# Optimization experiments

Hardware: AMD Instinct MI355X
Metric: run time of the kernel (lower is better)

## Reference

```python
import jax, jax.numpy as jnp
import numpy as np

N = 10000
E = 320000
IN = 10000
HID = 128
NCLS = 2


def setup_inputs() -> dict:
    key = jax.random.key(0)
    ks = jax.random.split(key, 8)
    x = jax.random.normal(ks[0], (N, IN), dtype=jnp.float32)
    edge_index = jax.random.randint(ks[1], (2, E), 0, N, dtype=jnp.int64)
    edge_weight = jax.random.uniform(ks[2], (E,), dtype=jnp.float32)
    # GCNConv linear (no bias folding issues: PyG GCNConv uses Linear(in, out, bias=False) + separate bias)
    W_conv = jax.random.normal(ks[3], (IN, HID), dtype=jnp.float32) / np.sqrt(IN)
    b_conv = jnp.zeros((HID,), dtype=jnp.float32)
    W_lin = jax.random.normal(ks[4], (HID, NCLS), dtype=jnp.float32) / np.sqrt(HID)
    b_lin = jnp.zeros((NCLS,), dtype=jnp.float32)
    return {"x": x, "edge_index": edge_index, "edge_weight": edge_weight,
            "W_conv": W_conv, "b_conv": b_conv, "W_lin": W_lin, "b_lin": b_lin}


def reference(x, edge_index, edge_weight, W_conv, b_conv, W_lin, b_lin):
    n = x.shape[0]
    row, col = edge_index[0], edge_index[1]
    # add self loops with weight 1 (GCNConv add_self_loops=True, fill_value=1.)
    loop = jnp.arange(n, dtype=row.dtype)
    row = jnp.concatenate([row, loop])
    col = jnp.concatenate([col, loop])
    ew = jnp.concatenate([edge_weight, jnp.ones((n,), dtype=edge_weight.dtype)])
    # symmetric GCN normalization: deg from destination (col) index
    deg = jax.ops.segment_sum(ew, col, num_segments=n)
    dinv = jnp.where(deg > 0, jax.lax.rsqrt(deg), 0.0)
    norm = dinv[row] * ew * dinv[col]  # [E+N]
    # linear transform then weighted scatter-add aggregation
    h = x @ W_conv                      # [N, HID]
    msg = norm[:, None] * h[row]        # [E+N, HID] gather on source nodes
    out = jax.ops.segment_sum(msg, col, num_segments=n) + b_conv  # [N, HID]
    out = jax.nn.relu(out)
    # dropout p=0.0 is identity
    logits = out @ W_lin + b_lin        # [N, 2]
    return jax.nn.softmax(logits, axis=1)
```

## Files before the change

### kernel.cpp

```cpp
#include <hip/hip_runtime.h>
#include <hip/hip_bf16.h>
#include <math.h>

#define NN   10000
#define NE   320000
#define KK   10000
#define HID  128
#define KPAD 10048
#define MT   79
#define KITERS 157
#define NSPLIT 8

typedef __bf16 bf16x8 __attribute__((ext_vector_type(8)));
typedef float  f32x16 __attribute__((ext_vector_type(16)));

#define OFF_DINV 0u
#define OFF_FLAG 40960u
#define OFF_CNT  45056u
#define OFF_ROW  86016u
#define OFF_CUR  126976u
#define OFF_ER   262144u
#define OFF_EC   1572864u
#define OFF_CSRS 2883584u
#define OFF_CSRW 4194304u
#define OFF_H    8388608u
#define OFF_WT   13631488u

__device__ inline unsigned short f2bf(float f) {
  unsigned int v = __builtin_bit_cast(unsigned int, f);
  unsigned int lsb = (v >> 16) & 1u;
  v += 0x7fffu + lsb;
  return (unsigned short)(v >> 16);
}

__global__ __launch_bounds__(64) void k_detect(const int* __restrict__ ei,
                                               int* __restrict__ flag) {
  int t = threadIdx.x;
  int v = ei[2*t + 1];
  unsigned long long b = __ballot(v != 0);
  if (t == 0) flag[0] = (b == 0ull) ? 1 : 0;
}

__global__ __launch_bounds__(256) void k_edges(const int* __restrict__ ei,
                                               const int* __restrict__ flag,
                                               int* __restrict__ er,
                                               int* __restrict__ ec) {
  int e = blockIdx.x*256 + threadIdx.x;
  if (e < NE) {
    int s = flag[0];
    er[e] = ei[(size_t)e << s];
    ec[e] = ei[((size_t)(NE + e)) << s];
  }
}

__global__ __launch_bounds__(256) void k_transpose(const float* __restrict__ W,
                                                   unsigned short* __restrict__ Wt) {
  __shared__ float t[32][33];
  const int tx = threadIdx.x, ty = threadIdx.y;
  const int bk = blockIdx.x, bn = blockIdx.y;
#pragma unroll
  for (int j = 0; j < 4; ++j) {
    int k = bk*32 + ty + j*8;
    int n = bn*32 + tx;
    float v = 0.0f;
    if (k < KK) v = W[(size_t)k*HID + n];
    t[ty + j*8][tx] = v;
  }
  __syncthreads();
#pragma unroll
  for (int j = 0; j < 4; ++j) {
    int n = bn*32 + ty + j*8;
    int k = bk*32 + tx;
    Wt[(size_t)n*KPAD + k] = f2bf(t[tx][ty + j*8]);
  }
}

__global__ __launch_bounds__(256) void k_deg(const int* __restrict__ ec,
                                             const float* __restrict__ ew,
                                             float* __restrict__ deg,
                                             int* __restrict__ cnt) {
  int e = blockIdx.x*256 + threadIdx.x;
  if (e < NE) {
    int c = ec[e];
    atomicAdd(&deg[c], ew[e]);
    atomicAdd(&cnt[c], 1);
  }
}

__global__ __launch_bounds__(256) void k_dinv(float* __restrict__ deg) {
  int i = blockIdx.x*256 + threadIdx.x;
  if (i < NN) {
    float d = deg[i] + 1.0f;
    deg[i] = (d > 0.0f) ? (1.0f / sqrtf(d)) : 0.0f;
  }
}

__global__ __launch_bounds__(256) void k_scan(const int* __restrict__ cnt,
                                              int* __restrict__ rowstart,
                                              int* __restrict__ cursor) {
  __shared__ int sums[256];
  const int t = threadIdx.x;
  const int CH = 40;
  const int base = t * CH;
  int s = 0;
  for (int k = 0; k < CH; ++k) {
    int i = base + k;
    if (i < NN) s += cnt[i];
  }
  sums[t] = s;
  __syncthreads();
  for (int off = 1; off < 256; off <<= 1) {
    int add = (t >= off) ? sums[t - off] : 0;
    __syncthreads();
    sums[t] += add;
    __syncthreads();
  }
  int run = (t == 0) ? 0 : sums[t - 1];
  for (int k = 0; k < CH; ++k) {
    int i = base + k;
    if (i < NN) {
      rowstart[i] = run;
      cursor[i]   = run;
      run += cnt[i];
    }
  }
  if (t == 255) rowstart[NN] = run;
}

__global__ __launch_bounds__(256) void k_scatter(const int* __restrict__ er,
                                                 const int* __restrict__ ec,
                                                 const float* __restrict__ ew,
                                                 const float* __restrict__ dinv,
                                                 int* __restrict__ cursor,
                                                 int* __restrict__ csr_src,
                                                 float* __restrict__ csr_w) {
  int e = blockIdx.x*256 + threadIdx.x;
  if (e < NE) {
    int r = er[e], c = ec[e];
    int slot = atomicAdd(&cursor[c], 1);
    csr_src[slot] = r;
    csr_w[slot]   = dinv[r] * ew[e] * dinv[c];
  }
}

__global__ __launch_bounds__(256) void k_gemm(const float* __restrict__ xg,
                                              const unsigned short* __restrict__ Wt,
                                              float* __restrict__ h) {
  __shared__ unsigned short lA[128*64];
  __shared__ unsigned short lB[128*64];
  const int tid  = threadIdx.x;
  const int lane = tid & 63;
  const int w    = tid >> 6;
  const int bid  = blockIdx.x;
  const int mt   = bid % MT;
  const int kc   = bid / MT;
  const int m0   = mt * 128;
  const int it0  = (KITERS * kc) / NSPLIT;
  const int it1  = (KITERS * (kc + 1)) / NSPLIT;

  const int srow = tid >> 3;
  const int scol = (tid & 7) * 8;
  const float* pA[4];
  const unsigned short* pB[4];
#pragma unroll
  for (int r = 0; r < 4; ++r) {
    int ga = m0 + r*32 + srow; if (ga > NN-1) ga = NN-1;
    pA[r] = xg + (size_t)ga * KK + scol;
    pB[r] = Wt + (size_t)(r*32 + srow) * KPAD + scol;
  }

  f32x16 acc[4];
#pragma unroll
  for (int ct = 0; ct < 4; ++ct)
#pragma unroll
    for (int q = 0; q < 16; ++q) acc[ct][q] = 0.0f;

  for (int it = it0; it < it1; ++it) {
    const int k0 = it * 64;
    __syncthreads();
#pragma unroll
    for (int r = 0; r < 4; ++r) {
      __builtin_amdgcn_global_load_lds(
          (const __attribute__((address_space(1))) unsigned int*)(pB[r] + k0),
          (__attribute__((address_space(3))) unsigned int*)(&lB[r*2048 + tid*8]),
          16, 0, 0);
    }
#pragma unroll
    for (int r = 0; r < 4; ++r) {
      float4 f0 = make_float4(0.f,0.f,0.f,0.f), f1 = f0;
      if ((k0 + scol) < KK) {
        f0 = *(const float4*)(pA[r] + k0);
        f1 = *(const float4*)(pA[r] + k0 + 4);
      }
      uint4 u;
      u.x = (unsigned)f2bf(f0.x) | ((unsigned)f2bf(f0.y) << 16);
      u.y = (unsigned)f2bf(f0.z) | ((unsigned)f2bf(f0.w) << 16);
      u.z = (unsigned)f2bf(f1.x) | ((unsigned)f2bf(f1.y) << 16);
      u.w = (unsigned)f2bf(f1.z) | ((unsigned)f2bf(f1.w) << 16);
      *((uint4*)&lA[r*2048 + tid*8]) = u;
    }
    __syncthreads();

    const unsigned short* Arow = &lA[(w*32 + (lane & 31))*64 + (lane >> 5)*8];
    const unsigned short* Brow = &lB[((lane & 31))*64 + (lane >> 5)*8];
#pragma unroll
    for (int s = 0; s < 4; ++s) {
      bf16x8 a = *(const bf16x8*)(Arow + s*16);
#pragma unroll
      for (int ct = 0; ct < 4; ++ct) {
        bf16x8 b = *(const bf16x8*)(Brow + ct*2048 + s*16);
        acc[ct] = __builtin_amdgcn_mfma_f32_32x32x16_bf16(a, b, acc[ct], 0, 0, 0);
      }
    }
  }

#pragma unroll
  for (int ct = 0; ct < 4; ++ct) {
    int col = ct*32 + (lane & 31);
#pragma unroll
    for (int reg = 0; reg < 16; ++reg) {
      int rloc = (reg & 3) + 8*(reg >> 2) + 4*(lane >> 5);
      int row = m0 + w*32 + rloc;
      if (row < NN) atomicAdd(&h[(size_t)row*HID + col], acc[ct][reg]);
    }
  }
}

__global__ __launch_bounds__(256) void k_aggout(const int* __restrict__ rowstart,
                                                const int* __restrict__ csr_src,
                                                const float* __restrict__ csr_w,
                                                const float* __restrict__ h,
                                                const float* __restrict__ dinv,
                                                const float* __restrict__ bc,
                                                const float* __restrict__ Wl,
                                                const float* __restrict__ bl,
                                                float* __restrict__ out) {
  int i = blockIdx.x*4 + (threadIdx.x >> 6);
  if (i >= NN) return;
  int lane = threadIdx.x & 63;
  const float* hp = h + 2*lane;
  int j  = rowstart[i];
  int j1 = rowstart[i + 1];

  float ax = 0.f, ay = 0.f;
  for (; j + 3 < j1; j += 4) {
    int   s0 = csr_src[j],   s1 = csr_src[j+1], s2 = csr_src[j+2], s3 = csr_src[j+3];
    float w0 = csr_w[j],     w1 = csr_w[j+1],   w2 = csr_w[j+2],   w3 = csr_w[j+3];
    float2 a = *(const float2*)(hp + (size_t)s0*HID);
    float2 b = *(const float2*)(hp + (size_t)s1*HID);
    float2 c = *(const float2*)(hp + (size_t)s2*HID);
    float2 d = *(const float2*)(hp + (size_t)s3*HID);
    ax += w0*a.x + w1*b.x + w2*c.x + w3*d.x;
    ay += w0*a.y + w1*b.y + w2*c.y + w3*d.y;
  }
  for (; j < j1; ++j) {
    int   s0 = csr_src[j];
    float w0 = csr_w[j];
    float2 a = *(const float2*)(hp + (size_t)s0*HID);
    ax += w0*a.x; ay += w0*a.y;
  }

  float di = dinv[i], d2 = di*di;
  float2 hs = *(const float2*)(hp + (size_t)i*HID);
  float2 bb = *(const float2*)(bc + 2*lane);
  float v0 = fmaxf(ax + d2*hs.x + bb.x, 0.0f);
  float v1 = fmaxf(ay + d2*hs.y + bb.y, 0.0f);

  float4 w4 = *(const float4*)(Wl + 4*lane);
  float l0 = v0*w4.x + v1*w4.z;
  float l1 = v0*w4.y + v1*w4.w;
#pragma unroll
  for (int off = 32; off > 0; off >>= 1) {
    l0 += __shfl_down(l0, off);
    l1 += __shfl_down(l1, off);
  }
  if (lane == 0) {
    l0 += bl[0]; l1 += bl[1];
    float m  = fmaxf(l0, l1);
    float e0 = expf(l0 - m), e1 = expf(l1 - m);
    float s  = 1.0f / (e0 + e1);
    *(float2*)(out + (size_t)i*2) = make_float2(e0 * s, e1 * s);
  }
}

extern "C" void kernel_launch(void* const* d_in, const int* in_sizes, int n_in,
                              void* d_out, int out_size, void* d_ws, size_t ws_size,
                              hipStream_t stream) {
  (void)in_sizes; (void)n_in; (void)out_size; (void)ws_size;
  const float* x  = (const float*)d_in[0];
  const int*   ei = (const int*)d_in[1];
  const float* ew = (const float*)d_in[2];
  const float* Wc = (const float*)d_in[3];
  const float* bc = (const float*)d_in[4];
  const float* Wl = (const float*)d_in[5];
  const float* bl = (const float*)d_in[6];

  char* ws = (char*)d_ws;
  float* dinv = (float*)(ws + OFF_DINV);
  int*   flag = (int*)(ws + OFF_FLAG);
  int*   cnt  = (int*)(ws + OFF_CNT);
  int*   row  = (int*)(ws + OFF_ROW);
  int*   cur  = (int*)(ws + OFF_CUR);
  int*   er   = (int*)(ws + OFF_ER);
  int*   ec   = (int*)(ws + OFF_EC);
  int*   csrs = (int*)(ws + OFF_CSRS);
  float* csrw = (float*)(ws + OFF_CSRW);
  float* h    = (float*)(ws + OFF_H);
  unsigned short* Wt = (unsigned short*)(ws + OFF_WT);
  float* out = (float*)d_out;

  hipMemsetAsync(dinv, 0, NN*sizeof(float), stream);
  hipMemsetAsync(cnt,  0, NN*sizeof(int),   stream);
  hipMemsetAsync(h,    0, (size_t)NN*HID*sizeof(float), stream);

  k_detect<<<1, 64, 0, stream>>>(ei, flag);
  k_edges <<<(NE + 255)/256, 256, 0, stream>>>(ei, flag, er, ec);
  k_transpose<<<dim3(KPAD/32, HID/32), dim3(32, 8), 0, stream>>>(Wc, Wt);
  k_deg <<<(NE + 255)/256, 256, 0, stream>>>(ec, ew, dinv, cnt);
  k_dinv<<<(NN + 255)/256, 256, 0, stream>>>(dinv);
  k_scan<<<1, 256, 0, stream>>>(cnt, row, cur);
  k_scatter<<<(NE + 255)/256, 256, 0, stream>>>(er, ec, ew, dinv, cur, csrs, csrw);
  k_gemm<<<MT*NSPLIT, 256, 0, stream>>>(x, Wt, h);
  k_aggout<<<NN/4, 256, 0, stream>>>(row, csrs, csrw, h, dinv, bc, Wl, bl, out);
}
```

Baseline: 692.3 us.

## Double-buffer GEMM LDS tiles and fuse degree counting into edge conversion

The GEMM main loop now uses two LDS buffers per operand. It issues the next tile's global loads (async LDS loads for B, register loads for A) before running the MFMAs on the current tile, so there is one barrier per iteration instead of two. Separately, the degree and count atomics move into the edge-conversion kernel, which removes one launch and one pass over the edge list. The trade-off is double the LDS use per block, which may lower occupancy, plus more registers to hold the prefetched A tile.

```diff
diff --git a/kernel.cpp b/kernel.cpp
--- a/kernel.cpp
+++ b/kernel.cpp
@@ -43,13 +43,20 @@
 
 __global__ __launch_bounds__(256) void k_edges(const int* __restrict__ ei,
                                                const int* __restrict__ flag,
+                                               const float* __restrict__ ew,
                                                int* __restrict__ er,
-                                               int* __restrict__ ec) {
+                                               int* __restrict__ ec,
+                                               float* __restrict__ deg,
+                                               int* __restrict__ cnt) {
   int e = blockIdx.x*256 + threadIdx.x;
   if (e < NE) {
     int s = flag[0];
-    er[e] = ei[(size_t)e << s];
-    ec[e] = ei[((size_t)(NE + e)) << s];
+    int r = ei[(size_t)e << s];
+    int c = ei[((size_t)(NE + e)) << s];
+    er[e] = r;
+    ec[e] = c;
+    atomicAdd(&deg[c], ew[e]);
+    atomicAdd(&cnt[c], 1);
   }
 }
 
@@ -72,18 +79,6 @@
     int n = bn*32 + ty + j*8;
     int k = bk*32 + tx;
     Wt[(size_t)n*KPAD + k] = f2bf(t[tx][ty + j*8]);
-  }
-}
-
-__global__ __launch_bounds__(256) void k_deg(const int* __restrict__ ec,
-                                             const float* __restrict__ ew,
-                                             float* __restrict__ deg,
-                                             int* __restrict__ cnt) {
-  int e = blockIdx.x*256 + threadIdx.x;
-  if (e < NE) {
-    int c = ec[e];
-    atomicAdd(&deg[c], ew[e]);
-    atomicAdd(&cnt[c], 1);
   }
 }
 
@@ -146,8 +141,8 @@
 __global__ __launch_bounds__(256) void k_gemm(const float* __restrict__ xg,
                                               const unsigned short* __restrict__ Wt,
                                               float* __restrict__ h) {
-  __shared__ unsigned short lA[128*64];
-  __shared__ unsigned short lB[128*64];
+  __shared__ unsigned short lA[2*128*64];
+  __shared__ unsigned short lB[2*128*64];
   const int tid  = threadIdx.x;
   const int lane = tid & 63;
   const int w    = tid >> 6;
@@ -175,34 +170,59 @@
 #pragma unroll
     for (int q = 0; q < 16; ++q) acc[ct][q] = 0.0f;
 
+  float4 fA[4][2];
+
+#define ISSUE_B(K0, SEL)                                                          \
+  _Pragma("unroll")                                                               \
+  for (int r = 0; r < 4; ++r) {                                                   \
+    __builtin_amdgcn_global_load_lds(                                             \
+        (const __attribute__((address_space(1))) unsigned int*)(pB[r] + (K0)),    \
+        (__attribute__((address_space(3))) unsigned int*)(&lB[(SEL)*8192 + r*2048 + tid*8]), \
+        16, 0, 0);                                                                \
+  }
+
+#define LOAD_A(K0)                                                                \
+  _Pragma("unroll")                                                               \
+  for (int r = 0; r < 4; ++r) {                                                   \
+    if (((K0) + scol) < KK) {                                                     \
+      fA[r][0] = *(const float4*)(pA[r] + (K0));                                  \
+      fA[r][1] = *(const float4*)(pA[r] + (K0) + 4);                              \
+    } else {                                                                      \
+      fA[r][0] = make_float4(0.f,0.f,0.f,0.f);                                    \
+      fA[r][1] = make_float4(0.f,0.f,0.f,0.f);                                    \
+    }                                                                             \
+  }
+
+#define WRITE_A(SEL)                                                              \
+  _Pragma("unroll")                                                               \
+  for (int r = 0; r < 4; ++r) {                                                   \
+    uint4 u;                                                                      \
+    u.x = (unsigned)f2bf(fA[r][0].x) | ((unsigned)f2bf(fA[r][0].y) << 16);        \
+    u.y = (unsigned)f2bf(fA[r][0].z) | ((unsigned)f2bf(fA[r][0].w) << 16);        \
+    u.z = (unsigned)f2bf(fA[r][1].x) | ((unsigned)f2bf(fA[r][1].y) << 16);        \
+    u.w = (unsigned)f2bf(fA[r][1].z) | ((unsigned)f2bf(fA[r][1].w) << 16);        \
+    *((uint4*)&lA[(SEL)*8192 + r*2048 + tid*8]) = u;                              \
+  }
+
+  {
+    const int k0 = it0 * 64;
+    ISSUE_B(k0, 0);
+    LOAD_A(k0);
+    WRITE_A(0);
+  }
+  __syncthreads();
+
   for (int it = it0; it < it1; ++it) {
-    const int k0 = it * 64;
-    __syncthreads();
-#pragma unroll
-    for (int r = 0; r < 4; ++r) {
-      __builtin_amdgcn_global_load_lds(
-          (const __attribute__((address_space(1))) unsigned int*)(pB[r] + k0),
-          (__attribute__((address_space(3))) unsigned int*)(&lB[r*2048 + tid*8]),
-          16, 0, 0);
+    const int cur = (it - it0) & 1;
+    const int nxt = cur ^ 1;
+    const bool more = (it + 1) < it1;
+    if (more) {
+      const int k0n = (it + 1) * 64;
+      ISSUE_B(k0n, nxt);
+      LOAD_A(k0n);
     }
-#pragma unroll
-    for (int r = 0; r < 4; ++r) {
-      float4 f0 = make_float4(0.f,0.f,0.f,0.f), f1 = f0;
-      if ((k0 + scol) < KK) {
-        f0 = *(const float4*)(pA[r] + k0);
-        f1 = *(const float4*)(pA[r] + k0 + 4);
-      }
-      uint4 u;
-      u.x = (unsigned)f2bf(f0.x) | ((unsigned)f2bf(f0.y) << 16);
-      u.y = (unsigned)f2bf(f0.z) | ((unsigned)f2bf(f0.w) << 16);
-      u.z = (unsigned)f2bf(f1.x) | ((unsigned)f2bf(f1.y) << 16);
-      u.w = (unsigned)f2bf(f1.z) | ((unsigned)f2bf(f1.w) << 16);
-      *((uint4*)&lA[r*2048 + tid*8]) = u;
-    }
-    __syncthreads();
-
-    const unsigned short* Arow = &lA[(w*32 + (lane & 31))*64 + (lane >> 5)*8];
-    const unsigned short* Brow = &lB[((lane & 31))*64 + (lane >> 5)*8];
+    const unsigned short* Arow = &lA[cur*8192 + (w*32 + (lane & 31))*64 + (lane >> 5)*8];
+    const unsigned short* Brow = &lB[cur*8192 + ((lane & 31))*64 + (lane >> 5)*8];
 #pragma unroll
     for (int s = 0; s < 4; ++s) {
       bf16x8 a = *(const bf16x8*)(Arow + s*16);
@@ -212,6 +232,8 @@
         acc[ct] = __builtin_amdgcn_mfma_f32_32x32x16_bf16(a, b, acc[ct], 0, 0, 0);
       }
     }
+    if (more) { WRITE_A(nxt); }
+    __syncthreads();
   }
 
 #pragma unroll
@@ -224,6 +246,9 @@
       if (row < NN) atomicAdd(&h[(size_t)row*HID + col], acc[ct][reg]);
     }
   }
+#undef ISSUE_B
+#undef LOAD_A
+#undef WRITE_A
 }
 
 __global__ __launch_bounds__(256) void k_aggout(const int* __restrict__ rowstart,
@@ -314,9 +339,8 @@
   hipMemsetAsync(h,    0, (size_t)NN*HID*sizeof(float), stream);
 
   k_detect<<<1, 64, 0, stream>>>(ei, flag);
-  k_edges <<<(NE + 255)/256, 256, 0, stream>>>(ei, flag, er, ec);
+  k_edges <<<(NE + 255)/256, 256, 0, stream>>>(ei, flag, ew, er, ec, dinv, cnt);
   k_transpose<<<dim3(KPAD/32, HID/32), dim3(32, 8), 0, stream>>>(Wc, Wt);
-  k_deg <<<(NE + 255)/256, 256, 0, stream>>>(ec, ew, dinv, cnt);
   k_dinv<<<(NN + 255)/256, 256, 0, stream>>>(dinv);
   k_scan<<<1, 256, 0, stream>>>(cnt, row, cur);
   k_scatter<<<(NE + 255)/256, 256, 0, stream>>>(er, ec, ew, dinv, cur, csrs, csrw);
```

Measured after the change: 763.1 us. 10.2% more time.

## Swizzle GEMM LDS tiles and fuse degree/dinv kernels into edge and scan passes

Applied to the files above, without the earlier changes.

The GEMM now stores A and B tiles in LDS with an XOR swizzle on the 16-byte chunk index, and reads them back through precomputed swizzled offsets. This is meant to cut LDS bank conflicts on the MFMA operand loads. Separately, the degree atomics move into the edge-extraction kernel and the rsqrt normalization moves into the single-block scan kernel, which removes two launches. The trade-off is that the dinv computation now runs in one block, and the atomics run in the same pass as the index extraction.

```diff
diff --git a/kernel.cpp b/kernel.cpp
--- a/kernel.cpp
+++ b/kernel.cpp
@@ -43,13 +43,20 @@
 
 __global__ __launch_bounds__(256) void k_edges(const int* __restrict__ ei,
                                                const int* __restrict__ flag,
+                                               const float* __restrict__ ew,
                                                int* __restrict__ er,
-                                               int* __restrict__ ec) {
+                                               int* __restrict__ ec,
+                                               float* __restrict__ deg,
+                                               int* __restrict__ cnt) {
   int e = blockIdx.x*256 + threadIdx.x;
   if (e < NE) {
     int s = flag[0];
-    er[e] = ei[(size_t)e << s];
-    ec[e] = ei[((size_t)(NE + e)) << s];
+    int r = ei[(size_t)e << s];
+    int c = ei[((size_t)(NE + e)) << s];
+    er[e] = r;
+    ec[e] = c;
+    atomicAdd(&deg[c], ew[e]);
+    atomicAdd(&cnt[c], 1);
   }
 }
 
@@ -75,33 +82,21 @@
   }
 }
 
-__global__ __launch_bounds__(256) void k_deg(const int* __restrict__ ec,
-                                             const float* __restrict__ ew,
-                                             float* __restrict__ deg,
-                                             int* __restrict__ cnt) {
-  int e = blockIdx.x*256 + threadIdx.x;
-  if (e < NE) {
-    int c = ec[e];
-    atomicAdd(&deg[c], ew[e]);
-    atomicAdd(&cnt[c], 1);
-  }
-}
-
-__global__ __launch_bounds__(256) void k_dinv(float* __restrict__ deg) {
-  int i = blockIdx.x*256 + threadIdx.x;
-  if (i < NN) {
-    float d = deg[i] + 1.0f;
-    deg[i] = (d > 0.0f) ? (1.0f / sqrtf(d)) : 0.0f;
-  }
-}
-
 __global__ __launch_bounds__(256) void k_scan(const int* __restrict__ cnt,
                                               int* __restrict__ rowstart,
-                                              int* __restrict__ cursor) {
+                                              int* __restrict__ cursor,
+                                              float* __restrict__ deg) {
   __shared__ int sums[256];
   const int t = threadIdx.x;
   const int CH = 40;
   const int base = t * CH;
+  for (int k = 0; k < CH; ++k) {
+    int i = base + k;
+    if (i < NN) {
+      float d = deg[i] + 1.0f;
+      deg[i] = (d > 0.0f) ? (1.0f / sqrtf(d)) : 0.0f;
+    }
+  }
   int s = 0;
   for (int k = 0; k < CH; ++k) {
     int i = base + k;
@@ -158,15 +153,18 @@
   const int it0  = (KITERS * kc) / NSPLIT;
   const int it1  = (KITERS * (kc + 1)) / NSPLIT;
 
-  const int srow = tid >> 3;
-  const int scol = (tid & 7) * 8;
+  const int srow  = tid >> 3;
+  const int chunk = tid & 7;
+  const int swz   = chunk ^ (srow & 7);
+  const int scol  = chunk * 8;
+
   const float* pA[4];
   const unsigned short* pB[4];
 #pragma unroll
   for (int r = 0; r < 4; ++r) {
     int ga = m0 + r*32 + srow; if (ga > NN-1) ga = NN-1;
     pA[r] = xg + (size_t)ga * KK + scol;
-    pB[r] = Wt + (size_t)(r*32 + srow) * KPAD + scol;
+    pB[r] = Wt + (size_t)(r*32 + srow) * KPAD + swz*8;
   }
 
   f32x16 acc[4];
@@ -174,6 +172,11 @@
   for (int ct = 0; ct < 4; ++ct)
 #pragma unroll
     for (int q = 0; q < 16; ++q) acc[ct][q] = 0.0f;
+
+  int co[4];
+#pragma unroll
+  for (int s = 0; s < 4; ++s)
+    co[s] = ((((lane >> 5) + 2*s) ^ (lane & 7)) << 3);
 
   for (int it = it0; it < it1; ++it) {
     const int k0 = it * 64;
@@ -197,18 +200,18 @@
       u.y = (unsigned)f2bf(f0.z) | ((unsigned)f2bf(f0.w) << 16);
       u.z = (unsigned)f2bf(f1.x) | ((unsigned)f2bf(f1.y) << 16);
       u.w = (unsigned)f2bf(f1.z) | ((unsigned)f2bf(f1.w) << 16);
-      *((uint4*)&lA[r*2048 + tid*8]) = u;
+      *((uint4*)&lA[(r*32 + srow)*64 + swz*8]) = u;
     }
     __syncthreads();
 
-    const unsigned short* Arow = &lA[(w*32 + (lane & 31))*64 + (lane >> 5)*8];
-    const unsigned short* Brow = &lB[((lane & 31))*64 + (lane >> 5)*8];
+    const unsigned short* Aband = &lA[(w*32 + (lane & 31))*64];
+    const unsigned short* Bband = &lB[(lane & 31)*64];
 #pragma unroll
     for (int s = 0; s < 4; ++s) {
-      bf16x8 a = *(const bf16x8*)(Arow + s*16);
+      bf16x8 a = *(const bf16x8*)(Aband + co[s]);
 #pragma unroll
       for (int ct = 0; ct < 4; ++ct) {
-        bf16x8 b = *(const bf16x8*)(Brow + ct*2048 + s*16);
+        bf16x8 b = *(const bf16x8*)(Bband + ct*2048 + co[s]);
         acc[ct] = __builtin_amdgcn_mfma_f32_32x32x16_bf16(a, b, acc[ct], 0, 0, 0);
       }
     }
@@ -314,11 +317,9 @@
   hipMemsetAsync(h,    0, (size_t)NN*HID*sizeof(float), stream);
 
   k_detect<<<1, 64, 0, stream>>>(ei, flag);
-  k_edges <<<(NE + 255)/256, 256, 0, stream>>>(ei, flag, er, ec);
+  k_edges <<<(NE + 255)/256, 256, 0, stream>>>(ei, flag, ew, er, ec, dinv, cnt);
   k_transpose<<<dim3(KPAD/32, HID/32), dim3(32, 8), 0, stream>>>(Wc, Wt);
-  k_deg <<<(NE + 255)/256, 256, 0, stream>>>(ec, ew, dinv, cnt);
-  k_dinv<<<(NN + 255)/256, 256, 0, stream>>>(dinv);
-  k_scan<<<1, 256, 0, stream>>>(cnt, row, cur);
+  k_scan<<<1, 256, 0, stream>>>(cnt, row, cur, dinv);
   k_scatter<<<(NE + 255)/256, 256, 0, stream>>>(er, ec, ew, dinv, cur, csrs, csrw);
   k_gemm<<<MT*NSPLIT, 256, 0, stream>>>(x, Wt, h);
   k_aggout<<<NN/4, 256, 0, stream>>>(row, csrs, csrw, h, dinv, bc, Wl, bl, out);
```

Result: no change. 696.5 us (+0.6%).
